# Kernel tuning notes

Measured on AMD Instinct MI355X. Metric: run time of the kernel, lower is better.

## Reference

```python
import jax, jax.numpy as jnp
import numpy as np

B, HRES, WRES, C, HEADS, WS, SS = 32, 64, 64, 256, 8, 8, 4
N = WS * WS
HID = 4 * C
EPS = 1e-5


def _rel_pos_index(ws):
    coords = np.stack(np.meshgrid(np.arange(ws), np.arange(ws), indexing='ij'))  # [2,ws,ws]
    cf = coords.reshape(2, -1)
    rel = (cf[:, :, None] - cf[:, None, :]).transpose(1, 2, 0)  # [N,N,2]
    rel[:, :, 0] += ws - 1
    rel[:, :, 1] += ws - 1
    rel[:, :, 0] *= 2 * ws - 1
    return rel.sum(-1).reshape(-1)  # [N*N]


def _attn_mask(H, W, ws, ss):
    img = np.zeros((H, W))
    cnt = 0
    for hs in (slice(0, -ws), slice(-ws, -ss), slice(-ss, None)):
        for wsl in (slice(0, -ws), slice(-ws, -ss), slice(-ss, None)):
            img[hs, wsl] = cnt
            cnt += 1
    mw = img.reshape(H // ws, ws, W // ws, ws).transpose(0, 2, 1, 3).reshape(-1, ws * ws)
    am = mw[:, None, :] - mw[:, :, None]  # [nW,N,N]
    return np.where(am != 0, -100.0, 0.0).astype(np.float32)


_RPI = jnp.asarray(_rel_pos_index(WS))
_MASK = jnp.asarray(_attn_mask(HRES, WRES, WS, SS))  # [nW,N,N]


def _ln(x, g, b):
    m = x.mean(-1, keepdims=True)
    v = ((x - m) ** 2).mean(-1, keepdims=True)
    return (x - m) / jnp.sqrt(v + EPS) * g + b


def setup_inputs() -> dict:
    key = jax.random.key(0)
    ks = jax.random.split(key, 16)
    s = 0.02
    return {
        'x': jax.random.normal(ks[0], (B, HRES * WRES, C), jnp.float32),
        'norm1_g': jnp.ones((C,), jnp.float32),
        'norm1_b': jnp.zeros((C,), jnp.float32),
        'qkv_w': jax.random.normal(ks[1], (3 * C, C), jnp.float32) * s,
        'qkv_b': jnp.zeros((3 * C,), jnp.float32),
        'rpb_table': jax.random.normal(ks[2], ((2 * WS - 1) ** 2, HEADS), jnp.float32) * s,
        'proj_w': jax.random.normal(ks[3], (C, C), jnp.float32) * s,
        'proj_b': jnp.zeros((C,), jnp.float32),
        'norm2_g': jnp.ones((C,), jnp.float32),
        'norm2_b': jnp.zeros((C,), jnp.float32),
        'fc1_w': jax.random.normal(ks[4], (HID, C), jnp.float32) * s,
        'fc1_b': jnp.zeros((HID,), jnp.float32),
        'fc2_w': jax.random.normal(ks[5], (C, HID), jnp.float32) * s,
        'fc2_b': jnp.zeros((C,), jnp.float32),
        'H': HRES,
        'W': WRES,
    }


def reference(x, norm1_g, norm1_b, qkv_w, qkv_b, rpb_table, proj_w, proj_b,
              norm2_g, norm2_b, fc1_w, fc1_b, fc2_w, fc2_b, H, W):
    Bn, L, Cd = x.shape
    ws, ss, nh = WS, SS, HEADS
    hd = Cd // nh
    shortcut = x
    h = _ln(x, norm1_g, norm1_b).reshape(Bn, H, W, Cd)
    # cyclic shift (H,W divisible by ws -> no padding needed)
    h = jnp.roll(h, (-ss, -ss), axis=(1, 2))
    # window partition: [B,H,W,C] -> [B*nW, N, C]
    h = h.reshape(Bn, H // ws, ws, W // ws, ws, Cd).transpose(0, 1, 3, 2, 4, 5).reshape(-1, N, Cd)
    qkv = (h @ qkv_w.T + qkv_b).reshape(-1, N, 3, nh, hd).transpose(2, 0, 3, 1, 4)
    q, k, v = qkv[0], qkv[1], qkv[2]  # [B_,h,N,d]
    attn = jnp.einsum('bhnd,bhmd->bhnm', q * (hd ** -0.5), k)
    rpb = rpb_table[_RPI].reshape(N, N, nh).transpose(2, 0, 1)  # [h,N,N]
    attn = attn + rpb[None]
    nW = _MASK.shape[0]
    attn = attn.reshape(Bn, nW, nh, N, N) + _MASK[None, :, None]
    attn = jax.nn.softmax(attn.reshape(-1, nh, N, N), axis=-1)
    o = jnp.einsum('bhnm,bhmd->bhnd', attn, v).transpose(0, 2, 1, 3).reshape(-1, N, Cd)
    o = o @ proj_w.T + proj_b
    # window reverse + reverse shift
    o = o.reshape(Bn, H // ws, W // ws, ws, ws, Cd).transpose(0, 1, 3, 2, 4, 5).reshape(Bn, H, W, Cd)
    o = jnp.roll(o, (ss, ss), axis=(1, 2)).reshape(Bn, L, Cd)
    x = shortcut + o
    h2 = _ln(x, norm2_g, norm2_b)
    h2 = jax.nn.gelu(h2 @ fc1_w.T + fc1_b, approximate=False)
    return x + (h2 @ fc2_w.T + fc2_b)
```

## Files before the change

### kernel.cpp

```cpp
#include <hip/hip_runtime.h>
#include <hip/hip_bf16.h>
#include <stdint.h>

typedef __bf16 bf16_t;
typedef __bf16 bf16x8 __attribute__((ext_vector_type(8)));
typedef __bf16 bf16x4 __attribute__((ext_vector_type(4)));
typedef float f32x4 __attribute__((ext_vector_type(4)));

#define MROWS 131072

__device__ __forceinline__ bf16_t to_bf16(float f) {
  __hip_bfloat16 h = __float2bfloat16(f);
  return *reinterpret_cast<bf16_t*>(&h);
}

__device__ __forceinline__ f32x4 mfma16(bf16x8 a, bf16x8 b, f32x4 c) {
  return __builtin_amdgcn_mfma_f32_16x16x32_bf16(a, b, c, 0, 0, 0);
}

__device__ __forceinline__ void gload16(const void* g, void* l) {
  __builtin_amdgcn_global_load_lds(
      (const __attribute__((address_space(1))) void*)g,
      (__attribute__((address_space(3))) void*)l, 16, 0, 0);
}

__device__ __forceinline__ int map_row(int m) {
  int b   = m >> 12;
  int rem = m & 4095;
  int win = rem >> 6;
  int n   = rem & 63;
  int gh  = ((win >> 3) << 3) + (n >> 3);
  int gw  = ((win & 7) << 3) + (n & 7);
  int sh  = (gh + 4) & 63;
  int sw  = (gw + 4) & 63;
  return (b << 12) + (sh << 6) + sw;
}

__global__ __launch_bounds__(256) void cvt_all(const float* __restrict__ qkv_w,
                                               const float* __restrict__ proj_w,
                                               const float* __restrict__ fc1_w,
                                               const float* __restrict__ fc2_w,
                                               bf16_t* __restrict__ qkv_o,
                                               bf16_t* __restrict__ proj_o,
                                               bf16_t* __restrict__ fc1_o,
                                               bf16_t* __restrict__ fc2_o) {
  int i = blockIdx.x * 256 + threadIdx.x;
  if (i < 196608)       qkv_o[i] = to_bf16(qkv_w[i]);
  else if (i < 262144)  proj_o[i - 196608] = to_bf16(proj_w[i - 196608]);
  else if (i < 524288)  fc1_o[i - 262144] = to_bf16(fc1_w[i - 262144]);
  else                  fc2_o[i - 524288] = to_bf16(fc2_w[i - 524288]);
}

__global__ __launch_bounds__(256) void bias_kernel(const float* __restrict__ rpbt,
                                                   float* __restrict__ bias) {
  int idx = blockIdx.x * 256 + threadIdx.x;
  int m = idx & 63, n = (idx >> 6) & 63, h = (idx >> 12) & 7, c = idx >> 15;
  int yn = n >> 3, xn = n & 7, ym = m >> 3, xm = m & 7;
  float v = rpbt[((yn - ym + 7) * 15 + (xn - xm + 7)) * 8 + h];
  int rn = (c & 2) ? (yn < 4 ? 1 : 2) : 0;
  int cn = (c & 1) ? (xn < 4 ? 1 : 2) : 0;
  int rm = (c & 2) ? (ym < 4 ? 1 : 2) : 0;
  int cm = (c & 1) ? (xm < 4 ? 1 : 2) : 0;
  if (rn * 3 + cn != rm * 3 + cm) v -= 100.0f;
  bias[idx] = v;
}

template <bool PERM>
__global__ __launch_bounds__(256) void ln_kernel(const float* __restrict__ xin,
                                                 const float* __restrict__ g,
                                                 const float* __restrict__ b,
                                                 bf16_t* __restrict__ out) {
  int row  = (blockIdx.x << 2) + (threadIdx.x >> 6);
  int lane = threadIdx.x & 63;
  int src  = PERM ? map_row(row) : row;
  float4 v = *reinterpret_cast<const float4*>(xin + (size_t)src * 256 + (lane << 2));
  float s = v.x + v.y + v.z + v.w;
#pragma unroll
  for (int d = 1; d < 64; d <<= 1) s += __shfl_xor(s, d);
  float mean = s * 0.00390625f;
  float ax = v.x - mean, ay = v.y - mean, az = v.z - mean, aw = v.w - mean;
  float s2 = ax * ax + ay * ay + az * az + aw * aw;
#pragma unroll
  for (int d = 1; d < 64; d <<= 1) s2 += __shfl_xor(s2, d);
  float rstd = rsqrtf(s2 * 0.00390625f + 1e-5f);
  float4 gv = *reinterpret_cast<const float4*>(g + (lane << 2));
  float4 bv = *reinterpret_cast<const float4*>(b + (lane << 2));
  bf16x4 o4;
  o4[0] = to_bf16(ax * rstd * gv.x + bv.x);
  o4[1] = to_bf16(ay * rstd * gv.y + bv.y);
  o4[2] = to_bf16(az * rstd * gv.z + bv.z);
  o4[3] = to_bf16(aw * rstd * gv.w + bv.w);
  *reinterpret_cast<bf16x4*>(out + (size_t)row * 256 + (lane << 2)) = o4;
}

template <int EPI>
__global__ __launch_bounds__(256) void gemm_bt(const bf16_t* __restrict__ A,
                                               const bf16_t* __restrict__ W,
                                               const float* __restrict__ bias,
                                               void* __restrict__ outp,
                                               void* __restrict__ outp2,
                                               void* __restrict__ outp3,
                                               const float* __restrict__ resid,
                                               int M, int N, int K, int NBN) {
  __shared__ __align__(16) bf16_t As[2][128 * 32];
  __shared__ __align__(16) bf16_t Bs[2][128 * 32];
  const int tid  = threadIdx.x;
  const int lane = tid & 63, lo = lane & 15, hi = lane >> 4;
  const int wave = tid >> 6;
  const int cpx = gridDim.x >> 3;
  const int wg  = (blockIdx.x & 7) * cpx + (blockIdx.x >> 3);
  const int bn = (wg % NBN) << 7, bm = (wg / NBN) << 7;
  const int wr = (wave >> 1) << 6, wc = (wave & 1) << 6;
  f32x4 acc[4][4] = {};

#define STAGE(buf, kt)                                                     \
  {                                                                        \
    int k0s = (kt) << 5;                                                   \
    _Pragma("unroll") for (int it = 0; it < 2; ++it) {                     \
      int ch = (it << 8) + tid;                                            \
      int r = ch >> 2, kf = (ch & 3) << 3;                                 \
      gload16(A + (size_t)(bm + r) * K + k0s + kf, &As[buf][ch << 3]);     \
      gload16(W + (size_t)(bn + r) * K + k0s + kf, &Bs[buf][ch << 3]);     \
    }                                                                      \
  }

  const int nt = K >> 5;
  STAGE(0, 0);
  __syncthreads();

  for (int t = 0; t < nt; ++t) {
    const int cur = t & 1;
    if (t + 1 < nt) STAGE(cur ^ 1, t + 1);
    bf16x8 af[4], bfr[4];
#pragma unroll
    for (int i = 0; i < 4; ++i)
      af[i] = *reinterpret_cast<const bf16x8*>(&As[cur][(wr + (i << 4) + lo) * 32 + (hi << 3)]);
#pragma unroll
    for (int j = 0; j < 4; ++j)
      bfr[j] = *reinterpret_cast<const bf16x8*>(&Bs[cur][(wc + (j << 4) + lo) * 32 + (hi << 3)]);
#pragma unroll
    for (int i = 0; i < 4; ++i)
#pragma unroll
      for (int j = 0; j < 4; ++j)
        acc[i][j] = mfma16(af[i], bfr[j], acc[i][j]);
    __syncthreads();
  }
#undef STAGE

  float bv[4];
#pragma unroll
  for (int j = 0; j < 4; ++j) bv[j] = bias[bn + wc + (j << 4) + lo];

#pragma unroll
  for (int i = 0; i < 4; ++i) {
#pragma unroll
    for (int r = 0; r < 4; ++r) {
      int row = bm + wr + (i << 4) + (hi << 2) + r;
      if constexpr (EPI == 2) {
        int xr = map_row(row);
        float* o = (float*)outp;
#pragma unroll
        for (int j = 0; j < 4; ++j) {
          int col = bn + wc + (j << 4) + lo;
          size_t idx = (size_t)xr * 256 + col;
          o[idx] = resid[idx] + acc[i][j][r] + bv[j];
        }
      } else if constexpr (EPI == 3) {
        float* o = (float*)outp;
#pragma unroll
        for (int j = 0; j < 4; ++j) {
          int col = bn + wc + (j << 4) + lo;
          size_t idx = (size_t)row * 256 + col;
          o[idx] = o[idx] + acc[i][j][r] + bv[j];
        }
      } else if constexpr (EPI == 4) {
#pragma unroll
        for (int j = 0; j < 4; ++j) {
          int col = bn + wc + (j << 4) + lo;
          bf16_t* base = (col < 256) ? (bf16_t*)outp
                        : (col < 512) ? (bf16_t*)outp2 : (bf16_t*)outp3;
          int hd = (col >> 5) & 7, d = col & 31;
          base[((size_t)hd * MROWS + row) * 32 + d] = to_bf16(acc[i][j][r] + bv[j]);
        }
      } else {
        bf16_t* o = (bf16_t*)outp;
#pragma unroll
        for (int j = 0; j < 4; ++j) {
          int col = bn + wc + (j << 4) + lo;
          float v = acc[i][j][r] + bv[j];
          if constexpr (EPI == 1) v = 0.5f * v * (1.0f + erff(v * 0.70710678118654752f));
          o[(size_t)row * N + col] = to_bf16(v);
        }
      }
    }
  }
}

__global__ __launch_bounds__(256) void attn_kernel(const bf16_t* __restrict__ qh,
                                                   const bf16_t* __restrict__ kh,
                                                   const bf16_t* __restrict__ vh,
                                                   const float* __restrict__ bias,
                                                   bf16_t* __restrict__ o) {
  __shared__ __align__(16) bf16_t Pl[4][64 * 72];
  __shared__ __align__(16) bf16_t Vt[4][32 * 72];
  const int wave = threadIdx.x >> 6, lane = threadIdx.x & 63;
  const int lo = lane & 15, hi = lane >> 4;
  const int id = (blockIdx.x << 2) + wave;
  const int win = id >> 3, h = id & 7;
  const size_t hb = ((size_t)h * MROWS + (size_t)win * 64) * 32;
  const bf16_t* qb = qh + hb;
  const bf16_t* kb = kh + hb;
  const bf16_t* vb = vh + hb;

  const bf16_t* vbl = vb + lane * 32;
#pragma unroll
  for (int c4 = 0; c4 < 4; ++c4) {
    bf16x8 v8 = *reinterpret_cast<const bf16x8*>(vbl + (c4 << 3));
#pragma unroll
    for (int e = 0; e < 8; ++e) Vt[wave][((c4 << 3) + e) * 72 + lane] = v8[e];
  }

  bf16x8 qa[4], ka[4];
#pragma unroll
  for (int i = 0; i < 4; ++i)
    qa[i] = *reinterpret_cast<const bf16x8*>(qb + ((i << 4) + lo) * 32 + (hi << 3));
#pragma unroll
  for (int j = 0; j < 4; ++j)
    ka[j] = *reinterpret_cast<const bf16x8*>(kb + ((j << 4) + lo) * 32 + (hi << 3));
  f32x4 s[4][4] = {};
#pragma unroll
  for (int i = 0; i < 4; ++i)
#pragma unroll
    for (int j = 0; j < 4; ++j) s[i][j] = mfma16(qa[i], ka[j], s[i][j]);

  const int wh = (win & 63) >> 3, ww = win & 7;
  const int cls = ((wh == 7) ? 2 : 0) + ((ww == 7) ? 1 : 0);
  const float* bb = bias + ((size_t)cls * 8 + h) * 4096;
  const float scale = 0.17677669529663687f;

  float pinv[4][4];
#pragma unroll
  for (int i = 0; i < 4; ++i) {
#pragma unroll
    for (int r = 0; r < 4; ++r) {
      int n = (i << 4) + (hi << 2) + r;
      const float* brow = bb + n * 64 + lo;
      float vals[4], mx = -1e30f;
#pragma unroll
      for (int j = 0; j < 4; ++j) {
        float val = s[i][j][r] * scale + brow[j << 4];
        vals[j] = val;
        mx = fmaxf(mx, val);
      }
#pragma unroll
      for (int d = 1; d < 16; d <<= 1) mx = fmaxf(mx, __shfl_xor(mx, d));
      float sum = 0.0f;
#pragma unroll
      for (int j = 0; j < 4; ++j) {
        float p = __expf(vals[j] - mx);
        sum += p;
        Pl[wave][n * 72 + (j << 4) + lo] = to_bf16(p);
      }
#pragma unroll
      for (int d = 1; d < 16; d <<= 1) sum += __shfl_xor(sum, d);
      pinv[i][r] = 1.0f / sum;
    }
  }

  __syncthreads();

  f32x4 oa[4][2] = {};
#pragma unroll
  for (int kt = 0; kt < 2; ++kt) {
    bf16x8 pa[4], va[2];
#pragma unroll
    for (int i = 0; i < 4; ++i)
      pa[i] = *reinterpret_cast<const bf16x8*>(&Pl[wave][((i << 4) + lo) * 72 + (kt << 5) + (hi << 3)]);
#pragma unroll
    for (int dt = 0; dt < 2; ++dt)
      va[dt] = *reinterpret_cast<const bf16x8*>(&Vt[wave][((dt << 4) + lo) * 72 + (kt << 5) + (hi << 3)]);
#pragma unroll
    for (int i = 0; i < 4; ++i)
#pragma unroll
      for (int dt = 0; dt < 2; ++dt) oa[i][dt] = mfma16(pa[i], va[dt], oa[i][dt]);
  }

  bf16_t* ob = o + (size_t)win * (64 * 256) + h * 32;
#pragma unroll
  for (int i = 0; i < 4; ++i)
#pragma unroll
    for (int r = 0; r < 4; ++r) {
      int n = (i << 4) + (hi << 2) + r;
      float piv = pinv[i][r];
#pragma unroll
      for (int dt = 0; dt < 2; ++dt)
        ob[(size_t)n * 256 + (dt << 4) + lo] = to_bf16(oa[i][dt][r] * piv);
    }
}

extern "C" void kernel_launch(void* const* d_in, const int* in_sizes, int n_in,
                              void* d_out, int out_size, void* d_ws, size_t ws_size,
                              hipStream_t stream) {
  const float* x      = (const float*)d_in[0];
  const float* n1g    = (const float*)d_in[1];
  const float* n1b    = (const float*)d_in[2];
  const float* qkv_w  = (const float*)d_in[3];
  const float* qkv_b  = (const float*)d_in[4];
  const float* rpbt   = (const float*)d_in[5];
  const float* proj_w = (const float*)d_in[6];
  const float* proj_b = (const float*)d_in[7];
  const float* n2g    = (const float*)d_in[8];
  const float* n2b    = (const float*)d_in[9];
  const float* fc1_w  = (const float*)d_in[10];
  const float* fc1_b  = (const float*)d_in[11];
  const float* fc2_w  = (const float*)d_in[12];
  const float* fc2_b  = (const float*)d_in[13];
  float* out = (float*)d_out;
  char*  ws  = (char*)d_ws;

  const size_t MB64 = 67108864;
  bf16_t* hln  = (bf16_t*)(ws);
  bf16_t* obuf = (bf16_t*)(ws);
  bf16_t* h2   = (bf16_t*)(ws);
  bf16_t* qbuf = (bf16_t*)(ws + MB64);
  bf16_t* x2n  = (bf16_t*)(ws + MB64);
  bf16_t* wb   = (bf16_t*)(ws + 2 * MB64);
  bf16_t* qkv_wb  = wb;
  bf16_t* proj_wb = qkv_wb + 196608;
  bf16_t* fc1_wb  = proj_wb + 65536;
  bf16_t* fc2_wb  = fc1_wb + 262144;
  float*  biast   = (float*)(fc2_wb + 262144);
  bf16_t* kbuf = (bf16_t*)d_out;
  bf16_t* vbuf = kbuf + 33554432;

  cvt_all<<<3072, 256, 0, stream>>>(qkv_w, proj_w, fc1_w, fc2_w,
                                    qkv_wb, proj_wb, fc1_wb, fc2_wb);
  bias_kernel<<<512, 256, 0, stream>>>(rpbt, biast);

  ln_kernel<true><<<32768, 256, 0, stream>>>(x, n1g, n1b, hln);

  gemm_bt<4><<<6144, 256, 0, stream>>>(hln, qkv_wb, qkv_b, qbuf, kbuf, vbuf,
                                       nullptr, MROWS, 768, 256, 6);

  attn_kernel<<<4096, 256, 0, stream>>>(qbuf, kbuf, vbuf, biast, obuf);

  gemm_bt<2><<<2048, 256, 0, stream>>>(obuf, proj_wb, proj_b, out, nullptr, nullptr,
                                       x, MROWS, 256, 256, 2);

  ln_kernel<false><<<32768, 256, 0, stream>>>(out, n2g, n2b, x2n);

  for (int c = 0; c < 4; ++c) {
    const bf16_t* xa = x2n + (size_t)c * 32768 * 256;
    gemm_bt<1><<<2048, 256, 0, stream>>>(xa, fc1_wb, fc1_b, h2, nullptr, nullptr,
                                         nullptr, 32768, 1024, 256, 8);
    gemm_bt<3><<<512, 256, 0, stream>>>(h2, fc2_wb, fc2_b, out + (size_t)c * 32768 * 256,
                                        nullptr, nullptr, nullptr, 32768, 256, 1024, 2);
  }
}
```

Before: 668.0 us.

## Use 256x256 swizzled-LDS GEMM tiles and fuse LayerNorm2 into projection epilogue

Replaces the 128x128, K=32 GEMM with a 512-thread 256x256 tile kernel that uses a K=64 step, XOR-swizzled LDS layout, dynamic shared memory and s_setprio around the MFMA block. The projection GEMM now covers the full 256-wide row, so it computes the residual sum and the row statistics for LayerNorm2 in its epilogue and writes x2n directly, removing the separate ln_kernel pass. The larger tiles raise data reuse and cut global traffic, but they raise register and LDS pressure and leave fewer blocks per launch, notably only 128 blocks for fc2. The fused LayerNorm computes variance as E[x^2]-mean^2, which is numerically less stable than the two-pass form it replaces.

```diff
diff --git a/kernel.cpp b/kernel.cpp
--- a/kernel.cpp
+++ b/kernel.cpp
@@ -94,105 +94,170 @@
 }
 
 template <int EPI>
-__global__ __launch_bounds__(256) void gemm_bt(const bf16_t* __restrict__ A,
+__global__ __launch_bounds__(512) void gemm256(const bf16_t* __restrict__ A,
                                                const bf16_t* __restrict__ W,
                                                const float* __restrict__ bias,
                                                void* __restrict__ outp,
                                                void* __restrict__ outp2,
                                                void* __restrict__ outp3,
                                                const float* __restrict__ resid,
+                                               const float* __restrict__ n2g,
+                                               const float* __restrict__ n2b,
+                                               bf16_t* __restrict__ x2n,
                                                int M, int N, int K, int NBN) {
-  __shared__ __align__(16) bf16_t As[2][128 * 32];
-  __shared__ __align__(16) bf16_t Bs[2][128 * 32];
+  extern __shared__ __align__(16) char smem[];
+  bf16_t* As  = (bf16_t*)smem;
+  bf16_t* Bs  = As + 2 * 16384;
+  float*  lnS = (float*)(Bs + 2 * 16384);
+  float*  lnQ = lnS + 1024;
+  float*  lnMR = lnQ + 1024;
   const int tid  = threadIdx.x;
   const int lane = tid & 63, lo = lane & 15, hi = lane >> 4;
-  const int wave = tid >> 6;
+  const int wid  = tid >> 6, wm = wid >> 2, wn = wid & 3;
   const int cpx = gridDim.x >> 3;
   const int wg  = (blockIdx.x & 7) * cpx + (blockIdx.x >> 3);
-  const int bn = (wg % NBN) << 7, bm = (wg / NBN) << 7;
-  const int wr = (wave >> 1) << 6, wc = (wave & 1) << 6;
-  f32x4 acc[4][4] = {};
-
-#define STAGE(buf, kt)                                                     \
-  {                                                                        \
-    int k0s = (kt) << 5;                                                   \
-    _Pragma("unroll") for (int it = 0; it < 2; ++it) {                     \
-      int ch = (it << 8) + tid;                                            \
-      int r = ch >> 2, kf = (ch & 3) << 3;                                 \
-      gload16(A + (size_t)(bm + r) * K + k0s + kf, &As[buf][ch << 3]);     \
-      gload16(W + (size_t)(bn + r) * K + k0s + kf, &Bs[buf][ch << 3]);     \
-    }                                                                      \
-  }
-
-  const int nt = K >> 5;
-  STAGE(0, 0);
-  __syncthreads();
-
-  for (int t = 0; t < nt; ++t) {
+  const int bn = (wg % NBN) << 8, bm = (wg / NBN) << 8;
+  f32x4 acc[8][4] = {};
+
+#define STAGE256(buf, kt)                                                      \
+  {                                                                            \
+    _Pragma("unroll") for (int l = 0; l < 4; ++l) {                            \
+      int ch = (l << 9) + tid;                                                 \
+      int row = ch >> 3, src = (ch & 7) ^ (row & 7);                           \
+      gload16(A + (size_t)(bm + row) * K + ((kt) << 6) + (src << 3),           \
+              &As[((buf) << 14) + (ch << 3)]);                                 \
+      gload16(W + (size_t)(bn + row) * K + ((kt) << 6) + (src << 3),           \
+              &Bs[((buf) << 14) + (ch << 3)]);                                 \
+    }                                                                          \
+  }
+
+  const int kt_n = K >> 6;
+  STAGE256(0, 0);
+  for (int t = 0; t < kt_n; ++t) {
     const int cur = t & 1;
-    if (t + 1 < nt) STAGE(cur ^ 1, t + 1);
-    bf16x8 af[4], bfr[4];
-#pragma unroll
-    for (int i = 0; i < 4; ++i)
-      af[i] = *reinterpret_cast<const bf16x8*>(&As[cur][(wr + (i << 4) + lo) * 32 + (hi << 3)]);
-#pragma unroll
-    for (int j = 0; j < 4; ++j)
-      bfr[j] = *reinterpret_cast<const bf16x8*>(&Bs[cur][(wc + (j << 4) + lo) * 32 + (hi << 3)]);
-#pragma unroll
-    for (int i = 0; i < 4; ++i)
-#pragma unroll
-      for (int j = 0; j < 4; ++j)
-        acc[i][j] = mfma16(af[i], bfr[j], acc[i][j]);
+    asm volatile("s_waitcnt vmcnt(0)" ::: "memory");
+    __builtin_amdgcn_s_barrier();
+    if (t + 1 < kt_n) STAGE256(cur ^ 1, t + 1);
+    const bf16_t* as = &As[cur << 14];
+    const bf16_t* bs = &Bs[cur << 14];
+    bf16x8 af[8][2], bfr[4][2];
+#pragma unroll
+    for (int mf = 0; mf < 8; ++mf)
+#pragma unroll
+      for (int kk = 0; kk < 2; ++kk) {
+        int row = (wm << 7) + (mf << 4) + lo;
+        int slot = ((kk << 2) + hi) ^ (row & 7);
+        af[mf][kk] = *reinterpret_cast<const bf16x8*>(&as[(row << 6) + (slot << 3)]);
+      }
+#pragma unroll
+    for (int nf = 0; nf < 4; ++nf)
+#pragma unroll
+      for (int kk = 0; kk < 2; ++kk) {
+        int row = (wn << 6) + (nf << 4) + lo;
+        int slot = ((kk << 2) + hi) ^ (row & 7);
+        bfr[nf][kk] = *reinterpret_cast<const bf16x8*>(&bs[(row << 6) + (slot << 3)]);
+      }
+    __builtin_amdgcn_s_setprio(1);
+#pragma unroll
+    for (int kk = 0; kk < 2; ++kk)
+#pragma unroll
+      for (int mf = 0; mf < 8; ++mf)
+#pragma unroll
+        for (int nf = 0; nf < 4; ++nf)
+          acc[mf][nf] = mfma16(af[mf][kk], bfr[nf][kk], acc[mf][nf]);
+    __builtin_amdgcn_s_setprio(0);
+  }
+#undef STAGE256
+
+  float bv4[4];
+#pragma unroll
+  for (int nf = 0; nf < 4; ++nf) bv4[nf] = bias[bn + (wn << 6) + (nf << 4) + lo];
+
+  if constexpr (EPI == 2) {
+    float* o = (float*)outp;
+    float gv[4], bnv[4];
+#pragma unroll
+    for (int nf = 0; nf < 4; ++nf) {
+      int col = bn + (wn << 6) + (nf << 4) + lo;
+      gv[nf] = n2g[col]; bnv[nf] = n2b[col];
+    }
+#pragma unroll
+    for (int mf = 0; mf < 8; ++mf)
+#pragma unroll
+      for (int r = 0; r < 4; ++r) {
+        int rl = (wm << 7) + (mf << 4) + (hi << 2) + r;
+        int xr = map_row(bm + rl);
+        float s = 0.f, q = 0.f;
+#pragma unroll
+        for (int nf = 0; nf < 4; ++nf) {
+          int col = bn + (wn << 6) + (nf << 4) + lo;
+          size_t idx = (size_t)xr * 256 + col;
+          float v = resid[idx] + acc[mf][nf][r] + bv4[nf];
+          acc[mf][nf][r] = v;
+          o[idx] = v;
+          s += v; q += v * v;
+        }
+#pragma unroll
+        for (int d = 1; d < 16; d <<= 1) { s += __shfl_xor(s, d); q += __shfl_xor(q, d); }
+        if (lo == 0) { lnS[(rl << 2) + wn] = s; lnQ[(rl << 2) + wn] = q; }
+      }
     __syncthreads();
-  }
-#undef STAGE
-
-  float bv[4];
-#pragma unroll
-  for (int j = 0; j < 4; ++j) bv[j] = bias[bn + wc + (j << 4) + lo];
-
-#pragma unroll
-  for (int i = 0; i < 4; ++i) {
-#pragma unroll
-    for (int r = 0; r < 4; ++r) {
-      int row = bm + wr + (i << 4) + (hi << 2) + r;
-      if constexpr (EPI == 2) {
-        int xr = map_row(row);
-        float* o = (float*)outp;
-#pragma unroll
-        for (int j = 0; j < 4; ++j) {
-          int col = bn + wc + (j << 4) + lo;
-          size_t idx = (size_t)xr * 256 + col;
-          o[idx] = resid[idx] + acc[i][j][r] + bv[j];
+    if (tid < 256) {
+      float s = lnS[tid << 2] + lnS[(tid << 2) + 1] + lnS[(tid << 2) + 2] + lnS[(tid << 2) + 3];
+      float q = lnQ[tid << 2] + lnQ[(tid << 2) + 1] + lnQ[(tid << 2) + 2] + lnQ[(tid << 2) + 3];
+      float mean = s * 0.00390625f;
+      float var  = q * 0.00390625f - mean * mean;
+      lnMR[tid << 1] = mean;
+      lnMR[(tid << 1) + 1] = rsqrtf(var + 1e-5f);
+    }
+    __syncthreads();
+#pragma unroll
+    for (int mf = 0; mf < 8; ++mf)
+#pragma unroll
+      for (int r = 0; r < 4; ++r) {
+        int rl = (wm << 7) + (mf << 4) + (hi << 2) + r;
+        int xr = map_row(bm + rl);
+        float mean = lnMR[rl << 1], rstd = lnMR[(rl << 1) + 1];
+#pragma unroll
+        for (int nf = 0; nf < 4; ++nf) {
+          int col = bn + (wn << 6) + (nf << 4) + lo;
+          x2n[(size_t)xr * 256 + col] = to_bf16((acc[mf][nf][r] - mean) * rstd * gv[nf] + bnv[nf]);
         }
-      } else if constexpr (EPI == 3) {
-        float* o = (float*)outp;
-#pragma unroll
-        for (int j = 0; j < 4; ++j) {
-          int col = bn + wc + (j << 4) + lo;
-          size_t idx = (size_t)row * 256 + col;
-          o[idx] = o[idx] + acc[i][j][r] + bv[j];
+      }
+  } else {
+#pragma unroll
+    for (int mf = 0; mf < 8; ++mf)
+#pragma unroll
+      for (int r = 0; r < 4; ++r) {
+        int row = bm + (wm << 7) + (mf << 4) + (hi << 2) + r;
+        if constexpr (EPI == 3) {
+          float* o = (float*)outp;
+#pragma unroll
+          for (int nf = 0; nf < 4; ++nf) {
+            int col = bn + (wn << 6) + (nf << 4) + lo;
+            size_t idx = (size_t)row * 256 + col;
+            o[idx] = o[idx] + acc[mf][nf][r] + bv4[nf];
+          }
+        } else if constexpr (EPI == 4) {
+#pragma unroll
+          for (int nf = 0; nf < 4; ++nf) {
+            int col = bn + (wn << 6) + (nf << 4) + lo;
+            bf16_t* base = (col < 256) ? (bf16_t*)outp
+                          : (col < 512) ? (bf16_t*)outp2 : (bf16_t*)outp3;
+            int hd = (col >> 5) & 7, d = col & 31;
+            base[((size_t)hd * MROWS + row) * 32 + d] = to_bf16(acc[mf][nf][r] + bv4[nf]);
+          }
+        } else {
+          bf16_t* o = (bf16_t*)outp;
+#pragma unroll
+          for (int nf = 0; nf < 4; ++nf) {
+            int col = bn + (wn << 6) + (nf << 4) + lo;
+            float v = acc[mf][nf][r] + bv4[nf];
+            if constexpr (EPI == 1) v = 0.5f * v * (1.0f + erff(v * 0.70710678118654752f));
+            o[(size_t)row * N + col] = to_bf16(v);
+          }
         }
-      } else if constexpr (EPI == 4) {
-#pragma unroll
-        for (int j = 0; j < 4; ++j) {
-          int col = bn + wc + (j << 4) + lo;
-          bf16_t* base = (col < 256) ? (bf16_t*)outp
-                        : (col < 512) ? (bf16_t*)outp2 : (bf16_t*)outp3;
-          int hd = (col >> 5) & 7, d = col & 31;
-          base[((size_t)hd * MROWS + row) * 32 + d] = to_bf16(acc[i][j][r] + bv[j]);
-        }
-      } else {
-        bf16_t* o = (bf16_t*)outp;
-#pragma unroll
-        for (int j = 0; j < 4; ++j) {
-          int col = bn + wc + (j << 4) + lo;
-          float v = acc[i][j][r] + bv[j];
-          if constexpr (EPI == 1) v = 0.5f * v * (1.0f + erff(v * 0.70710678118654752f));
-          o[(size_t)row * N + col] = to_bf16(v);
-        }
-      }
-    }
+      }
   }
 }
 
@@ -333,27 +398,39 @@
   bf16_t* kbuf = (bf16_t*)d_out;
   bf16_t* vbuf = kbuf + 33554432;
 
+  const int SMEM_G = 131072;
+  const int SMEM_P = 141312;
+  hipFuncSetAttribute(reinterpret_cast<const void*>(gemm256<1>),
+                      hipFuncAttributeMaxDynamicSharedMemorySize, SMEM_G);
+  hipFuncSetAttribute(reinterpret_cast<const void*>(gemm256<2>),
+                      hipFuncAttributeMaxDynamicSharedMemorySize, SMEM_P);
+  hipFuncSetAttribute(reinterpret_cast<const void*>(gemm256<3>),
+                      hipFuncAttributeMaxDynamicSharedMemorySize, SMEM_G);
+  hipFuncSetAttribute(reinterpret_cast<const void*>(gemm256<4>),
+                      hipFuncAttributeMaxDynamicSharedMemorySize, SMEM_G);
+
   cvt_all<<<3072, 256, 0, stream>>>(qkv_w, proj_w, fc1_w, fc2_w,
                                     qkv_wb, proj_wb, fc1_wb, fc2_wb);
   bias_kernel<<<512, 256, 0, stream>>>(rpbt, biast);
 
   ln_kernel<true><<<32768, 256, 0, stream>>>(x, n1g, n1b, hln);
 
-  gemm_bt<4><<<6144, 256, 0, stream>>>(hln, qkv_wb, qkv_b, qbuf, kbuf, vbuf,
-                                       nullptr, MROWS, 768, 256, 6);
+  gemm256<4><<<1536, 512, SMEM_G, stream>>>(hln, qkv_wb, qkv_b, qbuf, kbuf, vbuf,
+                                            nullptr, nullptr, nullptr, nullptr,
+                                            MROWS, 768, 256, 3);
 
   attn_kernel<<<4096, 256, 0, stream>>>(qbuf, kbuf, vbuf, biast, obuf);
 
-  gemm_bt<2><<<2048, 256, 0, stream>>>(obuf, proj_wb, proj_b, out, nullptr, nullptr,
-                                       x, MROWS, 256, 256, 2);
-
-  ln_kernel<false><<<32768, 256, 0, stream>>>(out, n2g, n2b, x2n);
+  gemm256<2><<<512, 512, SMEM_P, stream>>>(obuf, proj_wb, proj_b, out, nullptr, nullptr,
+                                           x, n2g, n2b, x2n, MROWS, 256, 256, 1);
 
   for (int c = 0; c < 4; ++c) {
     const bf16_t* xa = x2n + (size_t)c * 32768 * 256;
-    gemm_bt<1><<<2048, 256, 0, stream>>>(xa, fc1_wb, fc1_b, h2, nullptr, nullptr,
-                                         nullptr, 32768, 1024, 256, 8);
-    gemm_bt<3><<<512, 256, 0, stream>>>(h2, fc2_wb, fc2_b, out + (size_t)c * 32768 * 256,
-                                        nullptr, nullptr, nullptr, 32768, 256, 1024, 2);
-  }
-}
+    gemm256<1><<<512, 512, SMEM_G, stream>>>(xa, fc1_wb, fc1_b, h2, nullptr, nullptr,
+                                             nullptr, nullptr, nullptr, nullptr,
+                                             32768, 1024, 256, 4);
+    gemm256<3><<<128, 512, SMEM_G, stream>>>(h2, fc2_wb, fc2_b, out + (size_t)c * 32768 * 256,
+                                             nullptr, nullptr, nullptr, nullptr, nullptr, nullptr,
+                                             32768, 256, 1024, 1);
+  }
+}
```

New measurement: 795.3 us. 19.1% more time.
